# Performance work log

Measured on AMD Instinct MI355X. Metric: run time of the kernel, lower is better.

## Reference

```python
import jax, jax.numpy as jnp
import numpy as np

B, T, Q = 64, 200, 4096


def setup_inputs() -> dict:
    key = jax.random.key(0)
    k1, k2, k3, k4 = jax.random.split(key, 4)
    # predictions in (0,1) like post-sigmoid model output
    pred = jax.random.uniform(k1, (B, T, Q), dtype=jnp.float32)
    # build one-hot interaction matrix: correct answers in [0:Q], incorrect in [Q:2Q]
    qids = jax.random.randint(k2, (B, T), 0, Q)
    correct = jax.random.randint(k3, (B, T), 0, 2)
    seqlen = jax.random.randint(k4, (B,), 2, T + 1)  # ragged true lengths
    valid = (jnp.arange(T)[None, :] < seqlen[:, None])
    slot = qids + Q * (1 - correct)  # index into 2Q one-hot
    batch = jax.nn.one_hot(slot, 2 * Q, dtype=jnp.float32) * valid[..., None]
    return {"pred": pred, "batch": batch, "isTest": 0, "testseqlen": 50}


def reference(pred, batch, isTest, testseqlen):
    Bb, Tt, Q2 = batch.shape
    Qn = Q2 // 2
    Tm1 = Tt - 1
    cor = batch[:, :, :Qn]
    inc = batch[:, :, Qn:]
    delta = cor + inc  # [B, T, Q] one-hot of attempted question
    # original: per-student [T-1,Q] @ [Q,T-1] matmul, then gather row-diagonal
    temp = jnp.einsum('btq,bsq->bts', pred[:, :Tm1], delta[:, 1:])  # [B,T-1,T-1]
    p = jnp.diagonal(temp, axis1=1, axis2=2)  # [B, T-1]
    flag = batch.sum(-1)[:, 1:]  # >0 where step is non-padding
    a = ((cor.sum(-1) - inc.sum(-1) + 1.0) // 2.0)[:, 1:]  # 1 correct, 0 else
    idx = jnp.arange(Tm1)
    # dynamic truncation: keep up to last non-padding step (or index 0)
    last = jnp.maximum(jnp.max(jnp.where(flag > 0, idx, -1), axis=1), 0)  # [B]
    start = jnp.zeros_like(last)
    if isTest:
        length = last + 1
        start = jnp.where(length > testseqlen, length - testseqlen, 0)
    mask = (idx[None, :] >= start[:, None]) & (idx[None, :] <= last[:, None])
    maskf = mask.astype(p.dtype)
    cnt = maskf.sum(axis=1)  # per-student truncated length
    # BCELoss with torch's log clamp at -100
    logp = jnp.maximum(jnp.log(p), -100.0)
    log1mp = jnp.maximum(jnp.log1p(-p), -100.0)
    bce = -(a * logp + (1.0 - a) * log1mp)
    loss = jnp.sum(jnp.sum(bce * maskf, axis=1) / cnt)  # sum of per-student means
    # ragged concat of (p, a) returned as masked padded arrays + mask
    return loss, p * maskf, a * maskf, mask
```

## Files before the change

kernel.cpp:

```cpp
#include <hip/hip_runtime.h>
#include <math.h>

#define PB 64
#define PT 200
#define PQ 4096
#define PTM1 199
#define NROWS (PB * PTM1)

__global__ __launch_bounds__(256) void row_reduce_kernel(
    const float* __restrict__ pred,
    const float* __restrict__ batch,
    float* __restrict__ p_ws,
    float* __restrict__ flag_ws,
    float* __restrict__ a_ws)
{
    const int wid = blockIdx.x * (blockDim.x >> 6) + (threadIdx.x >> 6);
    if (wid >= NROWS) return;
    const int lane = threadIdx.x & 63;
    const int b  = wid / PTM1;
    const int tm = wid - b * PTM1;
    const int t  = tm + 1;

    const float4* row4 = (const float4*)(batch + ((size_t)(b * PT + t)) * (2 * PQ));

    float sc = 0.0f;
    float si = 0.0f;
    float w  = 0.0f;
    const float jb = (float)(4 * lane);

    #pragma unroll
    for (int k = 0; k < 16; ++k) {
        const float4 c = row4[lane + 64 * k];
        const float s4 = (c.x + c.y) + (c.z + c.w);
        sc += s4;
        const float jk = jb + (float)(256 * k);
        w += jk * s4 + (c.y + 2.0f * c.z + 3.0f * c.w);
    }
    #pragma unroll
    for (int k = 16; k < 32; ++k) {
        const float4 c = row4[lane + 64 * k];
        const float s4 = (c.x + c.y) + (c.z + c.w);
        si += s4;
        const float jk = jb + (float)(256 * k);
        w += jk * s4 + (c.y + 2.0f * c.z + 3.0f * c.w);
    }

    for (int off = 32; off > 0; off >>= 1) {
        sc += __shfl_down(sc, off);
        si += __shfl_down(si, off);
        w  += __shfl_down(w,  off);
    }

    if (lane == 0) {
        const int o = b * PTM1 + tm;
        const float flag = sc + si;
        flag_ws[o] = flag;
        a_ws[o] = floorf((sc - si + 1.0f) * 0.5f);
        float p = 0.0f;
        if (flag > 0.0f) {
            int idx = (int)(w + 0.5f);
            if (idx >= PQ) idx -= PQ;
            p = pred[((size_t)(b * PT + tm)) * PQ + idx];
        }
        p_ws[o] = p;
    }
}

__global__ __launch_bounds__(256) void finalize_kernel(
    const float* __restrict__ p_ws,
    const float* __restrict__ flag_ws,
    const float* __restrict__ a_ws,
    const int* __restrict__ isTest,
    const int* __restrict__ testseqlen,
    float* __restrict__ out,
    float* __restrict__ loss_ws)
{
    const int b = blockIdx.x;

    int mylast = -1;
    for (int t = threadIdx.x; t < PTM1; t += blockDim.x) {
        if (flag_ws[b * PTM1 + t] > 0.0f) mylast = max(mylast, t);
    }
    for (int off = 32; off > 0; off >>= 1)
        mylast = max(mylast, __shfl_down(mylast, off));
    __shared__ int swl[4];
    __shared__ int s_last;
    const int lane = threadIdx.x & 63;
    const int wv   = threadIdx.x >> 6;
    if (lane == 0) swl[wv] = mylast;
    __syncthreads();
    if (threadIdx.x == 0)
        s_last = max(max(swl[0], swl[1]), max(swl[2], swl[3]));
    __syncthreads();

    const int last = max(s_last, 0);
    int start = 0;
    if (isTest[0]) {
        const int length = last + 1;
        const int tl = testseqlen[0];
        if (length > tl) start = length - tl;
    }
    const float cnt = (float)(last - start + 1);

    float* out_p = out + 1;
    float* out_a = out + 1 + (size_t)PB * PTM1;
    float* out_m = out + 1 + (size_t)2 * PB * PTM1;

    float lsum = 0.0f;
    for (int t = threadIdx.x; t < PTM1; t += blockDim.x) {
        const int o = b * PTM1 + t;
        const bool m = (t >= start) && (t <= last);
        const float p = p_ws[o];
        const float a = a_ws[o];
        out_p[o] = m ? p : 0.0f;
        out_a[o] = m ? a : 0.0f;
        out_m[o] = m ? 1.0f : 0.0f;
        if (m) {
            const float logp  = fmaxf(logf(p), -100.0f);
            const float l1mp  = fmaxf(log1pf(-p), -100.0f);
            lsum += -(a * logp + (1.0f - a) * l1mp);
        }
    }
    for (int off = 32; off > 0; off >>= 1)
        lsum += __shfl_down(lsum, off);
    __shared__ float swf[4];
    if (lane == 0) swf[wv] = lsum;
    __syncthreads();
    if (threadIdx.x == 0) {
        lsum = swf[0] + swf[1] + swf[2] + swf[3];
        loss_ws[b] = lsum / cnt;
    }
}

__global__ __launch_bounds__(64) void loss_sum_kernel(
    const float* __restrict__ loss_ws, float* __restrict__ out)
{
    float v = loss_ws[threadIdx.x];
    for (int off = 32; off > 0; off >>= 1)
        v += __shfl_down(v, off);
    if (threadIdx.x == 0) out[0] = v;
}

extern "C" void kernel_launch(void* const* d_in, const int* in_sizes, int n_in,
                              void* d_out, int out_size, void* d_ws, size_t ws_size,
                              hipStream_t stream) {
    const float* pred  = (const float*)d_in[0];
    const float* batch = (const float*)d_in[1];
    const int* isTest     = (const int*)d_in[2];
    const int* testseqlen = (const int*)d_in[3];
    float* out = (float*)d_out;

    float* p_ws    = (float*)d_ws;
    float* flag_ws = p_ws + (size_t)PB * PTM1;
    float* a_ws    = flag_ws + (size_t)PB * PTM1;
    float* loss_ws = a_ws + (size_t)PB * PTM1;

    const int nblocks = (NROWS + 3) / 4;
    row_reduce_kernel<<<nblocks, 256, 0, stream>>>(pred, batch, p_ws, flag_ws, a_ws);
    finalize_kernel<<<PB, 256, 0, stream>>>(p_ws, flag_ws, a_ws, isTest, testseqlen,
                                            out, loss_ws);
    loss_sum_kernel<<<1, 64, 0, stream>>>(loss_ws, out);
}
```

Before: 613.4 us.

## Use nontemporal loads, ballot-based one-hot extraction, and fuse finalize with loss sum

The row scan now reads the interaction matrix with nontemporal vector loads. The three cross-lane shuffle reductions are replaced by a ballot: the single lane holding the one-hot entry writes flag, answer and gathered prediction directly. This relies on each row having at most one nonzero entry, so a row with two nonzeros would give a wrong or racy result. The per-student finalize kernel and the final loss-sum kernel are merged into one 1024-thread block that loops over students, dropping a launch at the cost of less parallelism in that stage.

```diff
diff --git a/kernel.cpp b/kernel.cpp
--- a/kernel.cpp
+++ b/kernel.cpp
@@ -7,6 +7,8 @@
 #define PTM1 199
 #define NROWS (PB * PTM1)
 
+typedef float f32x4 __attribute__((ext_vector_type(4)));
+
 __global__ __launch_bounds__(256) void row_reduce_kernel(
     const float* __restrict__ pred,
     const float* __restrict__ batch,
@@ -14,14 +16,14 @@
     float* __restrict__ flag_ws,
     float* __restrict__ a_ws)
 {
-    const int wid = blockIdx.x * (blockDim.x >> 6) + (threadIdx.x >> 6);
+    const int wid  = blockIdx.x * 4 + (threadIdx.x >> 6);
     if (wid >= NROWS) return;
     const int lane = threadIdx.x & 63;
     const int b  = wid / PTM1;
     const int tm = wid - b * PTM1;
     const int t  = tm + 1;
 
-    const float4* row4 = (const float4*)(batch + ((size_t)(b * PT + t)) * (2 * PQ));
+    const f32x4* row4 = (const f32x4*)(batch + ((size_t)(b * PT + t)) * (2 * PQ));
 
     float sc = 0.0f;
     float si = 0.0f;
@@ -30,115 +32,99 @@
 
     #pragma unroll
     for (int k = 0; k < 16; ++k) {
-        const float4 c = row4[lane + 64 * k];
-        const float s4 = (c.x + c.y) + (c.z + c.w);
+        const f32x4 c = __builtin_nontemporal_load(&row4[lane + 64 * k]);
+        const float s4 = (c[0] + c[1]) + (c[2] + c[3]);
         sc += s4;
-        const float jk = jb + (float)(256 * k);
-        w += jk * s4 + (c.y + 2.0f * c.z + 3.0f * c.w);
+        w += (jb + (float)(256 * k)) * s4 + (c[1] + 2.0f * c[2] + 3.0f * c[3]);
     }
     #pragma unroll
     for (int k = 16; k < 32; ++k) {
-        const float4 c = row4[lane + 64 * k];
-        const float s4 = (c.x + c.y) + (c.z + c.w);
+        const f32x4 c = __builtin_nontemporal_load(&row4[lane + 64 * k]);
+        const float s4 = (c[0] + c[1]) + (c[2] + c[3]);
         si += s4;
-        const float jk = jb + (float)(256 * k);
-        w += jk * s4 + (c.y + 2.0f * c.z + 3.0f * c.w);
+        w += (jb + (float)(256 * k)) * s4 + (c[1] + 2.0f * c[2] + 3.0f * c[3]);
     }
 
-    for (int off = 32; off > 0; off >>= 1) {
-        sc += __shfl_down(sc, off);
-        si += __shfl_down(si, off);
-        w  += __shfl_down(w,  off);
-    }
-
-    if (lane == 0) {
-        const int o = b * PTM1 + tm;
-        const float flag = sc + si;
-        flag_ws[o] = flag;
-        a_ws[o] = floorf((sc - si + 1.0f) * 0.5f);
-        float p = 0.0f;
-        if (flag > 0.0f) {
-            int idx = (int)(w + 0.5f);
-            if (idx >= PQ) idx -= PQ;
-            p = pred[((size_t)(b * PT + tm)) * PQ + idx];
+    const float me = sc + si;
+    const unsigned long long nz = __ballot(me != 0.0f);
+    const int o = b * PTM1 + tm;
+    if (nz == 0ULL) {
+        if (lane == 0) {
+            flag_ws[o] = 0.0f;
+            a_ws[o]    = 0.0f;
+            p_ws[o]    = 0.0f;
         }
-        p_ws[o] = p;
+    } else if (me != 0.0f) {
+        flag_ws[o] = me;
+        a_ws[o]    = sc;
+        int idx = (int)(w + 0.5f);
+        if (idx >= PQ) idx -= PQ;
+        p_ws[o] = pred[((size_t)(b * PT + tm)) * PQ + idx];
     }
 }
 
-__global__ __launch_bounds__(256) void finalize_kernel(
+__global__ __launch_bounds__(1024) void finalize_all_kernel(
     const float* __restrict__ p_ws,
     const float* __restrict__ flag_ws,
     const float* __restrict__ a_ws,
     const int* __restrict__ isTest,
     const int* __restrict__ testseqlen,
-    float* __restrict__ out,
-    float* __restrict__ loss_ws)
+    float* __restrict__ out)
 {
-    const int b = blockIdx.x;
-
-    int mylast = -1;
-    for (int t = threadIdx.x; t < PTM1; t += blockDim.x) {
-        if (flag_ws[b * PTM1 + t] > 0.0f) mylast = max(mylast, t);
-    }
-    for (int off = 32; off > 0; off >>= 1)
-        mylast = max(mylast, __shfl_down(mylast, off));
-    __shared__ int swl[4];
-    __shared__ int s_last;
     const int lane = threadIdx.x & 63;
     const int wv   = threadIdx.x >> 6;
-    if (lane == 0) swl[wv] = mylast;
-    __syncthreads();
-    if (threadIdx.x == 0)
-        s_last = max(max(swl[0], swl[1]), max(swl[2], swl[3]));
-    __syncthreads();
-
-    const int last = max(s_last, 0);
-    int start = 0;
-    if (isTest[0]) {
-        const int length = last + 1;
-        const int tl = testseqlen[0];
-        if (length > tl) start = length - tl;
-    }
-    const float cnt = (float)(last - start + 1);
+    __shared__ float s_loss[PB];
 
     float* out_p = out + 1;
     float* out_a = out + 1 + (size_t)PB * PTM1;
     float* out_m = out + 1 + (size_t)2 * PB * PTM1;
 
-    float lsum = 0.0f;
-    for (int t = threadIdx.x; t < PTM1; t += blockDim.x) {
-        const int o = b * PTM1 + t;
-        const bool m = (t >= start) && (t <= last);
-        const float p = p_ws[o];
-        const float a = a_ws[o];
-        out_p[o] = m ? p : 0.0f;
-        out_a[o] = m ? a : 0.0f;
-        out_m[o] = m ? 1.0f : 0.0f;
-        if (m) {
-            const float logp  = fmaxf(logf(p), -100.0f);
-            const float l1mp  = fmaxf(log1pf(-p), -100.0f);
-            lsum += -(a * logp + (1.0f - a) * l1mp);
+    const int istest = isTest[0];
+    const int tl     = testseqlen[0];
+
+    for (int b = wv; b < PB; b += 16) {
+        int mylast = -1;
+        for (int t = lane; t < PTM1; t += 64)
+            if (flag_ws[b * PTM1 + t] > 0.0f) mylast = max(mylast, t);
+        for (int off = 32; off > 0; off >>= 1)
+            mylast = max(mylast, __shfl_down(mylast, off));
+        int last = __shfl(mylast, 0);
+        last = max(last, 0);
+
+        int start = 0;
+        if (istest) {
+            const int length = last + 1;
+            if (length > tl) start = length - tl;
         }
+        const float cnt = (float)(last - start + 1);
+
+        float lsum = 0.0f;
+        for (int t = lane; t < PTM1; t += 64) {
+            const int o = b * PTM1 + t;
+            const bool m = (t >= start) && (t <= last);
+            const float p = p_ws[o];
+            const float a = a_ws[o];
+            out_p[o] = m ? p : 0.0f;
+            out_a[o] = m ? a : 0.0f;
+            out_m[o] = m ? 1.0f : 0.0f;
+            if (m) {
+                const float logp = fmaxf(logf(p), -100.0f);
+                const float l1mp = fmaxf(log1pf(-p), -100.0f);
+                lsum += -(a * logp + (1.0f - a) * l1mp);
+            }
+        }
+        for (int off = 32; off > 0; off >>= 1)
+            lsum += __shfl_down(lsum, off);
+        if (lane == 0) s_loss[b] = lsum / cnt;
     }
-    for (int off = 32; off > 0; off >>= 1)
-        lsum += __shfl_down(lsum, off);
-    __shared__ float swf[4];
-    if (lane == 0) swf[wv] = lsum;
     __syncthreads();
-    if (threadIdx.x == 0) {
-        lsum = swf[0] + swf[1] + swf[2] + swf[3];
-        loss_ws[b] = lsum / cnt;
+
+    if (wv == 0) {
+        float v = s_loss[lane];
+        for (int off = 32; off > 0; off >>= 1)
+            v += __shfl_down(v, off);
+        if (lane == 0) out[0] = v;
     }
-}
-
-__global__ __launch_bounds__(64) void loss_sum_kernel(
-    const float* __restrict__ loss_ws, float* __restrict__ out)
-{
-    float v = loss_ws[threadIdx.x];
-    for (int off = 32; off > 0; off >>= 1)
-        v += __shfl_down(v, off);
-    if (threadIdx.x == 0) out[0] = v;
 }
 
 extern "C" void kernel_launch(void* const* d_in, const int* in_sizes, int n_in,
@@ -153,11 +139,7 @@
     float* p_ws    = (float*)d_ws;
     float* flag_ws = p_ws + (size_t)PB * PTM1;
     float* a_ws    = flag_ws + (size_t)PB * PTM1;
-    float* loss_ws = a_ws + (size_t)PB * PTM1;
 
-    const int nblocks = (NROWS + 3) / 4;
-    row_reduce_kernel<<<nblocks, 256, 0, stream>>>(pred, batch, p_ws, flag_ws, a_ws);
-    finalize_kernel<<<PB, 256, 0, stream>>>(p_ws, flag_ws, a_ws, isTest, testseqlen,
-                                            out, loss_ws);
-    loss_sum_kernel<<<1, 64, 0, stream>>>(loss_ws, out);
+    row_reduce_kernel<<<NROWS / 4, 256, 0, stream>>>(pred, batch, p_ws, flag_ws, a_ws);
+    finalize_all_kernel<<<1, 1024, 0, stream>>>(p_ws, flag_ws, a_ws, isTest, testseqlen, out);
 }
```

Result: no change. 602.2 us (-1.8%).
